# Kernel optimization log

Measured on AMD Instinct MI355X. Metric: run time of the kernel, lower is better.

The kernel has to match this reference:

```python
import jax, jax.numpy as jnp
import numpy as np

N = 4096
IN_F = 256
F = 64      # out_features
H = 4       # heads
NEG_SLOPE = 0.2


def setup_inputs() -> dict:
    key = jax.random.key(0)
    k1, k2, k3, k4 = jax.random.split(key, 4)
    x = jax.random.normal(k1, (N, IN_F), dtype=jnp.float32)
    # symmetric random binary adjacency with self-loops (avoids empty softmax rows)
    adj = jax.random.bernoulli(k2, 0.5, (N, N)).astype(jnp.float32)
    adj = jnp.clip(adj + adj.T, 0.0, 1.0)
    adj = jnp.maximum(adj, jnp.eye(N, dtype=jnp.float32))
    W = jax.random.normal(k3, (IN_F, F * H), dtype=jnp.float32) * (1.0 / np.sqrt(IN_F))
    a = jax.random.normal(k4, (2 * F, 1), dtype=jnp.float32) * 0.1
    return {"x": x, "adj": adj, "W": W, "a": a}


def reference(x, adj, W, a):
    # h: [N, H, F]
    h = (x @ W).reshape(N, H, F)
    # e[i, j, h] = leakyrelu(a_l . h[i, h] + a_r . h[j, h])  -- avoids the O(N^2*H*2F) concat
    a_l = a[:F, 0]
    a_r = a[F:, 0]
    el = jnp.einsum('nhf,f->nh', h, a_l)  # [N, H]
    er = jnp.einsum('nhf,f->nh', h, a_r)  # [N, H]
    e = jax.nn.leaky_relu(el[:, None, :] + er[None, :, :], NEG_SLOPE)  # [N, N, H]
    e = jnp.where(adj[:, :, None] == 0, -jnp.inf, e)
    attention = jax.nn.softmax(e, axis=1)  # softmax over neighbors j
    h_prime = jnp.einsum('ijh,jhf->ihf', attention, h)  # [N, H, F]
    return h_prime.mean(axis=1)  # [N, F]  (heads > 1 -> mean over heads)
```

## Files before the change

kernel.cpp:

```cpp
#include <hip/hip_runtime.h>
#include <hip/hip_bf16.h>

#define NN 4096
#define LOG2E 1.44269504088896340736f

typedef __attribute__((ext_vector_type(8))) short s8v;
typedef __attribute__((ext_vector_type(4))) float f4v;

__device__ __forceinline__ unsigned fu(float x){ union{float f;unsigned u;}z; z.f=x; return z.u; }
__device__ __forceinline__ unsigned short f2bf_rne(float x){
  unsigned u = fu(x);
  u += 0x7fffu + ((u >> 16) & 1u);
  return (unsigned short)(u >> 16);
}
__device__ __forceinline__ unsigned pack2_rne(float a, float b){
  return (unsigned)f2bf_rne(a) | ((unsigned)f2bf_rne(b) << 16);
}

__global__ __launch_bounds__(256) void k1_proj(
    const float* __restrict__ x, const float* __restrict__ W,
    const float* __restrict__ a, unsigned short* __restrict__ Vf,
    float* __restrict__ el4, float* __restrict__ Qr, float* __restrict__ Sr)
{
  __shared__ float4 xs[512];
  const int t = threadIdx.x;
  const int r0 = blockIdx.x * 8;
  const float4* xg = (const float4*)(x + (size_t)r0 * 256);
  xs[t] = xg[t];
  xs[t + 256] = xg[t + 256];
  __syncthreads();

  float acc[8] = {0.f,0.f,0.f,0.f,0.f,0.f,0.f,0.f};
  const float* Wp = W + t;
  float w0 = Wp[0], w1 = Wp[256], w2 = Wp[512], w3 = Wp[768];
  #pragma unroll 1
  for (int k4 = 0; k4 < 64; ++k4) {
    const int kn = (k4 + 1) & 63;
    float nw0 = Wp[kn*1024 +   0];
    float nw1 = Wp[kn*1024 + 256];
    float nw2 = Wp[kn*1024 + 512];
    float nw3 = Wp[kn*1024 + 768];
    #pragma unroll
    for (int r = 0; r < 8; ++r) {
      float4 xv = xs[r*64 + k4];
      acc[r] = fmaf(xv.x, w0, acc[r]);
      acc[r] = fmaf(xv.y, w1, acc[r]);
      acc[r] = fmaf(xv.z, w2, acc[r]);
      acc[r] = fmaf(xv.w, w3, acc[r]);
    }
    w0 = nw0; w1 = nw1; w2 = nw2; w3 = nw3;
  }

  union { unsigned u[4]; s8v v; } pk;
  #pragma unroll
  for (int p = 0; p < 4; ++p)
    pk.u[p] = pack2_rne(acc[2*p], acc[2*p+1]);
  {
    const int hh = t >> 6, nf = (t >> 4) & 3, mm = t & 15;
    const int jblk = r0 >> 5, qq = (r0 >> 3) & 3;
    const size_t chunk = (size_t)(((hh * 128 + jblk) * 4 + nf) * 64 + qq * 16 + mm);
    *(s8v*)(Vf + chunk * 8) = pk.v;
  }

  const int f = t & 63, h = t >> 6;
  const float al = a[f], ar = a[64 + f];
  #pragma unroll
  for (int r = 0; r < 8; ++r) {
    float v = acc[r] * al;
    float u = acc[r] * ar;
    #pragma unroll
    for (int off = 32; off > 0; off >>= 1) {
      v += __shfl_xor(v, off);
      u += __shfl_xor(u, off);
    }
    if (f == 0) {
      el4[(r0 + r) * 4 + h] = v * LOG2E;
      float up = u * LOG2E;
      Qr[h * NN + (r0 + r)] = __builtin_amdgcn_exp2f(up);
      Sr[h * NN + (r0 + r)] = __builtin_amdgcn_exp2f(0.2f * up);
    }
  }
}

__global__ __launch_bounds__(256, 4) void k0_pack(
    const float* __restrict__ adj, const float* __restrict__ el4,
    const float* __restrict__ Qr, const float* __restrict__ Sr,
    unsigned long long* __restrict__ adjB,
    float* __restrict__ PL, float* __restrict__ RL)
{
  const int t = threadIdx.x;
  const int w = t >> 6, l = t & 63;
  const int row = blockIdx.x * 4 + w;
  const float* arow = adj + (size_t)row * NN;

  float4 elv = *(const float4*)(el4 + row * 4);
  const float P[4] = { __builtin_amdgcn_exp2f(elv.x), __builtin_amdgcn_exp2f(elv.y),
                       __builtin_amdgcn_exp2f(elv.z), __builtin_amdgcn_exp2f(elv.w) };
  const float R[4] = { __builtin_amdgcn_exp2f(0.2f*elv.x), __builtin_amdgcn_exp2f(0.2f*elv.y),
                       __builtin_amdgcn_exp2f(0.2f*elv.z), __builtin_amdgcn_exp2f(0.2f*elv.w) };
  float lsum[4] = {0.f, 0.f, 0.f, 0.f};

  float4 av, qv0, qv1, qv2, qv3, sv0, sv1, sv2, sv3;
  av  = *(const float4*)(arow + l * 4);
  qv0 = *(const float4*)(Qr + 0 * NN + l * 4);
  qv1 = *(const float4*)(Qr + 1 * NN + l * 4);
  qv2 = *(const float4*)(Qr + 2 * NN + l * 4);
  qv3 = *(const float4*)(Qr + 3 * NN + l * 4);
  sv0 = *(const float4*)(Sr + 0 * NN + l * 4);
  sv1 = *(const float4*)(Sr + 1 * NN + l * 4);
  sv2 = *(const float4*)(Sr + 2 * NN + l * 4);
  sv3 = *(const float4*)(Sr + 3 * NN + l * 4);

  #pragma unroll 1
  for (int p = 0; p < 16; ++p) {
    const int nb = ((p < 15) ? (p + 1) * 256 : 0) + l * 4;
    float4 nav  = *(const float4*)(arow + nb);
    float4 nqv0 = *(const float4*)(Qr + 0 * NN + nb);
    float4 nqv1 = *(const float4*)(Qr + 1 * NN + nb);
    float4 nqv2 = *(const float4*)(Qr + 2 * NN + nb);
    float4 nqv3 = *(const float4*)(Qr + 3 * NN + nb);
    float4 nsv0 = *(const float4*)(Sr + 0 * NN + nb);
    float4 nsv1 = *(const float4*)(Sr + 1 * NN + nb);
    float4 nsv2 = *(const float4*)(Sr + 2 * NN + nb);
    float4 nsv3 = *(const float4*)(Sr + 3 * NN + nb);

    unsigned long long b0 = __ballot(av.x != 0.0f);
    unsigned long long b1 = __ballot(av.y != 0.0f);
    unsigned long long b2 = __ballot(av.z != 0.0f);
    unsigned long long b3 = __ballot(av.w != 0.0f);
    if (l == 0) {
      unsigned long long* dst = adjB + (size_t)row * 64 + p * 4;
      dst[0] = b0; dst[1] = b1; dst[2] = b2; dst[3] = b3;
    }
    #pragma unroll
    for (int h = 0; h < 4; ++h) {
      const float4 qv = (h==0)?qv0:(h==1)?qv1:(h==2)?qv2:qv3;
      const float4 sv = (h==0)?sv0:(h==1)?sv1:(h==2)?sv2:sv3;
      float m0 = fmaxf(P[h] * qv.x, R[h] * sv.x);
      float m1 = fmaxf(P[h] * qv.y, R[h] * sv.y);
      float m2 = fmaxf(P[h] * qv.z, R[h] * sv.z);
      float m3 = fmaxf(P[h] * qv.w, R[h] * sv.w);
      lsum[h] = fmaf(av.x, m0, lsum[h]);
      lsum[h] = fmaf(av.y, m1, lsum[h]);
      lsum[h] = fmaf(av.z, m2, lsum[h]);
      lsum[h] = fmaf(av.w, m3, lsum[h]);
    }
    av = nav;
    qv0 = nqv0; qv1 = nqv1; qv2 = nqv2; qv3 = nqv3;
    sv0 = nsv0; sv1 = nsv1; sv2 = nsv2; sv3 = nsv3;
  }

  #pragma unroll
  for (int h = 0; h < 4; ++h) {
    float v = lsum[h];
    #pragma unroll
    for (int off = 32; off > 0; off >>= 1) v += __shfl_xor(v, off);
    lsum[h] = v;
  }
  if (l < 4) {
    float li = 1.0f / lsum[l];
    PL[row * 4 + l] = P[l] * li;
    RL[row * 4 + l] = R[l] * li;
  }
}

__global__ __launch_bounds__(256, 4) void k2_attn(
    const unsigned long long* __restrict__ adjB, const unsigned short* __restrict__ Vf,
    const float* __restrict__ PL, const float* __restrict__ RL,
    const float* __restrict__ Qr, const float* __restrict__ Sr,
    float* __restrict__ out)
{
  __shared__ float qs[8192];
  const int t = threadIdx.x;
  const int w = t >> 6, l = t & 63;
  const int m = l & 15, q = l >> 4;
  const int i0 = blockIdx.x * 16;
  const int sw = blockIdx.y * 4 + w;
  const int i = i0 + m;
  const int jwin = sw * 256;

  {
    const int jc = l >> 3, qq = (l >> 1) & 3, hp = (l & 1) * 4;
    #pragma unroll
    for (int h = 0; h < 4; ++h) {
      float4 qv = *(const float4*)(Qr + h * NN + jwin + l * 4);
      float4 sv = *(const float4*)(Sr + h * NN + jwin + l * 4);
      float* cell = qs + (((w * 4 + h) * 8 + jc) * 4 + qq) * 16;
      *(float4*)(cell + hp) = qv;
      *(float4*)(cell + 8 + hp) = sv;
    }
  }

  float4 pl4 = *(const float4*)(PL + i * 4);
  float4 rl4 = *(const float4*)(RL + i * 4);
  const float Pl[4] = {pl4.x, pl4.y, pl4.z, pl4.w};
  const float Rl[4] = {rl4.x, rl4.y, rl4.z, rl4.w};

  const unsigned long long* bp = adjB + (size_t)i * 64 + sw * 4;
  unsigned long long b0 = bp[0], b1 = bp[1], b2 = bp[2], b3 = bp[3];

  f4v acc[4];
  #pragma unroll
  for (int nf = 0; nf < 4; ++nf) acc[nf] = (f4v){0.f, 0.f, 0.f, 0.f};

  const s8v* vfp = (const s8v*)Vf;
  s8v Bc[4];
  #pragma unroll
  for (int nf = 0; nf < 4; ++nf)
    Bc[nf] = vfp[(size_t)((0 * 128 + sw * 8 + 0) * 4 + nf) * 64 + l];

  #pragma unroll 1
  for (int jc = 0; jc < 8; ++jc) {
    const unsigned sh = jc * 8 + q * 2;
    const unsigned t0 = (unsigned)(b0 >> sh) & 3u;
    const unsigned t1 = (unsigned)(b1 >> sh) & 3u;
    const unsigned t2 = (unsigned)(b2 >> sh) & 3u;
    const unsigned t3 = (unsigned)(b3 >> sh) & 3u;
    float bitf[8];
    bitf[0] = (float)(t0 & 1u); bitf[4] = (float)(t0 >> 1);
    bitf[1] = (float)(t1 & 1u); bitf[5] = (float)(t1 >> 1);
    bitf[2] = (float)(t2 & 1u); bitf[6] = (float)(t2 >> 1);
    bitf[3] = (float)(t3 & 1u); bitf[7] = (float)(t3 >> 1);

    #pragma unroll
    for (int h = 0; h < 4; ++h) {
      const int hn = (h < 3) ? h + 1 : 0;
      const int jcn = (h < 3) ? jc : jc + 1;
      s8v Bn[4];
      #pragma unroll
      for (int nf = 0; nf < 4; ++nf)
        Bn[nf] = vfp[(size_t)((hn * 128 + sw * 8 + jcn) * 4 + nf) * 64 + l];

      const float* cell = qs + (((w * 4 + h) * 8 + jc) * 4 + q) * 16;
      float4 q0  = *(const float4*)(cell);
      float4 q1  = *(const float4*)(cell + 4);
      float4 sv0 = *(const float4*)(cell + 8);
      float4 sv1 = *(const float4*)(cell + 12);
      const float Ph = Pl[h], Rh = Rl[h];
      float s0 = bitf[0] * fmaxf(Ph * q0.x, Rh * sv0.x);
      float s1 = bitf[1] * fmaxf(Ph * q0.y, Rh * sv0.y);
      float s2 = bitf[2] * fmaxf(Ph * q0.z, Rh * sv0.z);
      float s3 = bitf[3] * fmaxf(Ph * q0.w, Rh * sv0.w);
      float s4 = bitf[4] * fmaxf(Ph * q1.x, Rh * sv1.x);
      float s5 = bitf[5] * fmaxf(Ph * q1.y, Rh * sv1.y);
      float s6 = bitf[6] * fmaxf(Ph * q1.z, Rh * sv1.z);
      float s7 = bitf[7] * fmaxf(Ph * q1.w, Rh * sv1.w);
      union { unsigned u[4]; s8v v; } A;
      A.u[0] = pack2_rne(s0, s1);
      A.u[1] = pack2_rne(s2, s3);
      A.u[2] = pack2_rne(s4, s5);
      A.u[3] = pack2_rne(s6, s7);
      #pragma unroll
      for (int nf = 0; nf < 4; ++nf)
        acc[nf] = __builtin_amdgcn_mfma_f32_16x16x32_bf16(A.v, Bc[nf], acc[nf], 0, 0, 0);
      #pragma unroll
      for (int nf = 0; nf < 4; ++nf) Bc[nf] = Bn[nf];
    }
  }

  __syncthreads();
  if (w > 0) {
    float* dst = qs + ((w - 1) * 64 + l) * 20;
    #pragma unroll
    for (int nf = 0; nf < 4; ++nf)
      *(f4v*)(dst + nf * 4) = acc[nf];
  }
  __syncthreads();
  if (w == 0) {
    const float* src = qs + l * 20;
    #pragma unroll
    for (int nf = 0; nf < 4; ++nf) {
      f4v s = acc[nf];
      s += *(const f4v*)(src +    0 + nf * 4);
      s += *(const f4v*)(src + 1280 + nf * 4);
      s += *(const f4v*)(src + 2560 + nf * 4);
      #pragma unroll
      for (int r = 0; r < 4; ++r) {
        int row = i0 + q * 4 + r;
        int col = nf * 16 + m;
        atomicAdd(&out[row * 64 + col], 0.25f * s[r]);
      }
    }
  }
}

extern "C" void kernel_launch(void* const* d_in, const int* in_sizes, int n_in,
                              void* d_out, int out_size, void* d_ws, size_t ws_size,
                              hipStream_t stream) {
  const float* x   = (const float*)d_in[0];
  const float* adj = (const float*)d_in[1];
  const float* W   = (const float*)d_in[2];
  const float* a   = (const float*)d_in[3];
  float* out = (float*)d_out;

  char* ws = (char*)d_ws;
  unsigned short* Vf = (unsigned short*)ws;
  float* el4 = (float*)(ws + (2u << 20));
  float* Qr  = (float*)(ws + (2u << 20) + (64u << 10));
  float* Sr  = (float*)(ws + (2u << 20) + (128u << 10));
  float* PLp = (float*)(ws + (2u << 20) + (192u << 10));
  float* RLp = (float*)(ws + (2u << 20) + (256u << 10));
  unsigned long long* adjB = (unsigned long long*)(ws + (2u << 20) + (320u << 10));

  hipMemsetAsync(out, 0, (size_t)out_size * sizeof(float), stream);
  k1_proj<<<512, 256, 0, stream>>>(x, W, a, Vf, el4, Qr, Sr);
  k0_pack<<<1024, 256, 0, stream>>>(adj, el4, Qr, Sr, adjB, PLp, RLp);
  k2_attn<<<dim3(256, 4), 256, 0, stream>>>(adjB, Vf, PLp, RLp, Qr, Sr, out);
}
```

Measured before the change: 174.3 us.

## Split adjacency pack over column windows with atomic row-sum accumulation

```diff
diff --git a/kernel.cpp b/kernel.cpp
--- a/kernel.cpp
+++ b/kernel.cpp
@@ -82,91 +82,74 @@
   }
 }
 
-__global__ __launch_bounds__(256, 4) void k0_pack(
+__global__ __launch_bounds__(256, 8) void k0_pack(
     const float* __restrict__ adj, const float* __restrict__ el4,
     const float* __restrict__ Qr, const float* __restrict__ Sr,
-    unsigned long long* __restrict__ adjB,
-    float* __restrict__ PL, float* __restrict__ RL)
+    unsigned long long* __restrict__ adjB, float* __restrict__ lsum)
 {
+  __shared__ float qsh[2048];
   const int t = threadIdx.x;
   const int w = t >> 6, l = t & 63;
+  const int p = blockIdx.y;
   const int row = blockIdx.x * 4 + w;
-  const float* arow = adj + (size_t)row * NN;
+  const int jwin = p * 256;
+
+  {
+    const int h = t >> 6;
+    float4 qv = *(const float4*)(Qr + h * NN + jwin + l * 4);
+    float4 sv = *(const float4*)(Sr + h * NN + jwin + l * 4);
+    *(float4*)(qsh + h * 256 + l * 4) = qv;
+    *(float4*)(qsh + 1024 + h * 256 + l * 4) = sv;
+  }
+
+  const float4 av = *(const float4*)(adj + (size_t)row * NN + jwin + l * 4);
+
+  unsigned long long b0 = __ballot(av.x != 0.0f);
+  unsigned long long b1 = __ballot(av.y != 0.0f);
+  unsigned long long b2 = __ballot(av.z != 0.0f);
+  unsigned long long b3 = __ballot(av.w != 0.0f);
+  if (l == 0) {
+    unsigned long long* dst = adjB + (size_t)row * 64 + p * 4;
+    dst[0] = b0; dst[1] = b1; dst[2] = b2; dst[3] = b3;
+  }
 
   float4 elv = *(const float4*)(el4 + row * 4);
   const float P[4] = { __builtin_amdgcn_exp2f(elv.x), __builtin_amdgcn_exp2f(elv.y),
                        __builtin_amdgcn_exp2f(elv.z), __builtin_amdgcn_exp2f(elv.w) };
   const float R[4] = { __builtin_amdgcn_exp2f(0.2f*elv.x), __builtin_amdgcn_exp2f(0.2f*elv.y),
                        __builtin_amdgcn_exp2f(0.2f*elv.z), __builtin_amdgcn_exp2f(0.2f*elv.w) };
-  float lsum[4] = {0.f, 0.f, 0.f, 0.f};
-
-  float4 av, qv0, qv1, qv2, qv3, sv0, sv1, sv2, sv3;
-  av  = *(const float4*)(arow + l * 4);
-  qv0 = *(const float4*)(Qr + 0 * NN + l * 4);
-  qv1 = *(const float4*)(Qr + 1 * NN + l * 4);
-  qv2 = *(const float4*)(Qr + 2 * NN + l * 4);
-  qv3 = *(const float4*)(Qr + 3 * NN + l * 4);
-  sv0 = *(const float4*)(Sr + 0 * NN + l * 4);
-  sv1 = *(const float4*)(Sr + 1 * NN + l * 4);
-  sv2 = *(const float4*)(Sr + 2 * NN + l * 4);
-  sv3 = *(const float4*)(Sr + 3 * NN + l * 4);
-
-  #pragma unroll 1
-  for (int p = 0; p < 16; ++p) {
-    const int nb = ((p < 15) ? (p + 1) * 256 : 0) + l * 4;
-    float4 nav  = *(const float4*)(arow + nb);
-    float4 nqv0 = *(const float4*)(Qr + 0 * NN + nb);
-    float4 nqv1 = *(const float4*)(Qr + 1 * NN + nb);
-    float4 nqv2 = *(const float4*)(Qr + 2 * NN + nb);
-    float4 nqv3 = *(const float4*)(Qr + 3 * NN + nb);
-    float4 nsv0 = *(const float4*)(Sr + 0 * NN + nb);
-    float4 nsv1 = *(const float4*)(Sr + 1 * NN + nb);
-    float4 nsv2 = *(const float4*)(Sr + 2 * NN + nb);
-    float4 nsv3 = *(const float4*)(Sr + 3 * NN + nb);
-
-    unsigned long long b0 = __ballot(av.x != 0.0f);
-    unsigned long long b1 = __ballot(av.y != 0.0f);
-    unsigned long long b2 = __ballot(av.z != 0.0f);
-    unsigned long long b3 = __ballot(av.w != 0.0f);
-    if (l == 0) {
-      unsigned long long* dst = adjB + (size_t)row * 64 + p * 4;
-      dst[0] = b0; dst[1] = b1; dst[2] = b2; dst[3] = b3;
-    }
-    #pragma unroll
-    for (int h = 0; h < 4; ++h) {
-      const float4 qv = (h==0)?qv0:(h==1)?qv1:(h==2)?qv2:qv3;
-      const float4 sv = (h==0)?sv0:(h==1)?sv1:(h==2)?sv2:sv3;
-      float m0 = fmaxf(P[h] * qv.x, R[h] * sv.x);
-      float m1 = fmaxf(P[h] * qv.y, R[h] * sv.y);
-      float m2 = fmaxf(P[h] * qv.z, R[h] * sv.z);
-      float m3 = fmaxf(P[h] * qv.w, R[h] * sv.w);
-      lsum[h] = fmaf(av.x, m0, lsum[h]);
-      lsum[h] = fmaf(av.y, m1, lsum[h]);
-      lsum[h] = fmaf(av.z, m2, lsum[h]);
-      lsum[h] = fmaf(av.w, m3, lsum[h]);
-    }
-    av = nav;
-    qv0 = nqv0; qv1 = nqv1; qv2 = nqv2; qv3 = nqv3;
-    sv0 = nsv0; sv1 = nsv1; sv2 = nsv2; sv3 = nsv3;
-  }
-
+
+  __syncthreads();
+
+  float ls[4];
   #pragma unroll
   for (int h = 0; h < 4; ++h) {
-    float v = lsum[h];
+    float4 qv = *(const float4*)(qsh + h * 256 + l * 4);
+    float4 sv = *(const float4*)(qsh + 1024 + h * 256 + l * 4);
+    float s;
+    s  = av.x * fmaxf(P[h] * qv.x, R[h] * sv.x);
+    s  = fmaf(av.y, fmaxf(P[h] * qv.y, R[h] * sv.y), s);
+    s  = fmaf(av.z, fmaxf(P[h] * qv.z, R[h] * sv.z), s);
+    s  = fmaf(av.w, fmaxf(P[h] * qv.w, R[h] * sv.w), s);
+    ls[h] = s;
+  }
+  #pragma unroll
+  for (int h = 0; h < 4; ++h) {
+    float v = ls[h];
     #pragma unroll
     for (int off = 32; off > 0; off >>= 1) v += __shfl_xor(v, off);
-    lsum[h] = v;
-  }
-  if (l < 4) {
-    float li = 1.0f / lsum[l];
-    PL[row * 4 + l] = P[l] * li;
-    RL[row * 4 + l] = R[l] * li;
+    ls[h] = v;
+  }
+  if (l == 0) {
+    #pragma unroll
+    for (int h = 0; h < 4; ++h)
+      atomicAdd(&lsum[row * 4 + h], ls[h]);
   }
 }
 
 __global__ __launch_bounds__(256, 4) void k2_attn(
     const unsigned long long* __restrict__ adjB, const unsigned short* __restrict__ Vf,
-    const float* __restrict__ PL, const float* __restrict__ RL,
+    const float* __restrict__ el4, const float* __restrict__ lsum,
     const float* __restrict__ Qr, const float* __restrict__ Sr,
     float* __restrict__ out)
 {
@@ -191,10 +174,19 @@
     }
   }
 
-  float4 pl4 = *(const float4*)(PL + i * 4);
-  float4 rl4 = *(const float4*)(RL + i * 4);
-  const float Pl[4] = {pl4.x, pl4.y, pl4.z, pl4.w};
-  const float Rl[4] = {rl4.x, rl4.y, rl4.z, rl4.w};
+  float4 elv = *(const float4*)(el4 + i * 4);
+  float4 ls4 = *(const float4*)(lsum + i * 4);
+  float Pl[4], Rl[4];
+  {
+    const float el_[4] = {elv.x, elv.y, elv.z, elv.w};
+    const float lv_[4] = {ls4.x, ls4.y, ls4.z, ls4.w};
+    #pragma unroll
+    for (int h = 0; h < 4; ++h) {
+      const float inv = 1.0f / lv_[h];
+      Pl[h] = __builtin_amdgcn_exp2f(el_[h]) * inv;
+      Rl[h] = __builtin_amdgcn_exp2f(0.2f * el_[h]) * inv;
+    }
+  }
 
   const unsigned long long* bp = adjB + (size_t)i * 64 + sw * 4;
   unsigned long long b0 = bp[0], b1 = bp[1], b2 = bp[2], b3 = bp[3];
@@ -298,12 +290,12 @@
   float* el4 = (float*)(ws + (2u << 20));
   float* Qr  = (float*)(ws + (2u << 20) + (64u << 10));
   float* Sr  = (float*)(ws + (2u << 20) + (128u << 10));
-  float* PLp = (float*)(ws + (2u << 20) + (192u << 10));
-  float* RLp = (float*)(ws + (2u << 20) + (256u << 10));
-  unsigned long long* adjB = (unsigned long long*)(ws + (2u << 20) + (320u << 10));
+  float* lsum= (float*)(ws + (2u << 20) + (192u << 10));
+  unsigned long long* adjB = (unsigned long long*)(ws + (2u << 20) + (256u << 10));
 
   hipMemsetAsync(out, 0, (size_t)out_size * sizeof(float), stream);
+  hipMemsetAsync(lsum, 0, NN * 4 * sizeof(float), stream);
   k1_proj<<<512, 256, 0, stream>>>(x, W, a, Vf, el4, Qr, Sr);
-  k0_pack<<<1024, 256, 0, stream>>>(adj, el4, Qr, Sr, adjB, PLp, RLp);
-  k2_attn<<<dim3(256, 4), 256, 0, stream>>>(adjB, Vf, PLp, RLp, Qr, Sr, out);
-}
+  k0_pack<<<dim3(1024, 16), 256, 0, stream>>>(adj, el4, Qr, Sr, adjB, lsum);
+  k2_attn<<<dim3(256, 4), 256, 0, stream>>>(adjB, Vf, el4, lsum, Qr, Sr, out);
+}
```

New measurement: 170.0 us. 1.03x faster.
